# Optimization experiments

Hardware: AMD Instinct MI355X
Metric: run time of the kernel (lower is better)

Reference implementation:

```python
import jax, jax.numpy as jnp
import numpy as np

N_NODES = 100000
N_EDGES = 1600000
IN_F, HID_F, OUT_F = 64, 64, 32


def setup_inputs() -> dict:
    key = jax.random.key(0)
    k = jax.random.split(key, 6)
    features = jax.random.normal(k[0], (N_NODES, IN_F), dtype=jnp.float32)
    src = jax.random.randint(k[1], (N_EDGES,), 0, N_NODES, dtype=jnp.int32)
    dst = jax.random.randint(k[2], (N_EDGES,), 0, N_NODES, dtype=jnp.int32)
    # Linear params (Kaiming-uniform-ish scale)
    W1 = jax.random.normal(k[3], (IN_F, HID_F), dtype=jnp.float32) / np.sqrt(IN_F)
    b1 = jnp.zeros((HID_F,), dtype=jnp.float32)
    W2 = jax.random.normal(k[4], (HID_F, OUT_F), dtype=jnp.float32) / np.sqrt(HID_F)
    b2 = jnp.zeros((OUT_F,), dtype=jnp.float32)
    return {"features": features, "src": src, "dst": dst,
            "W1": W1, "b1": b1, "W2": W2, "b2": b2}


def _graph_conv(src, dst, n_nodes, h, W, b):
    # copy_u + sum: scatter-add source features into destination nodes (SpMM)
    agg = jax.ops.segment_sum(h[src], dst, num_segments=n_nodes)
    return agg @ W + b


def reference(features, src, dst, W1, b1, W2, b2):
    n = features.shape[0]
    h = jax.nn.relu(_graph_conv(src, dst, n, features, W1, b1))
    h = _graph_conv(src, dst, n, h, W2, b2)
    return h
```

## Files before the change

kernel.cpp:

```cpp
#include <hip/hip_runtime.h>

#define N_NODES 100000
#define N_EDGES 1600000
#define NB 782
#define CAP 3072
#define EPB 8192
#define NP1 196
#define CVB 200
#define YP 72
#define AP 72

typedef __attribute__((ext_vector_type(8))) short bhalf8;
typedef __attribute__((ext_vector_type(4))) float f32x4;

__device__ __forceinline__ unsigned short bf16r(float f) {
    unsigned u = __float_as_uint(f);
    unsigned r = (u >> 16) & 1;
    return (unsigned short)((u + 0x7fffu + r) >> 16);
}
__device__ __forceinline__ unsigned pk2(float a, float b) {
    return (unsigned)bf16r(a) | ((unsigned)bf16r(b) << 16);
}
__device__ __forceinline__ float bl(unsigned u) { return __uint_as_float(u << 16); }
__device__ __forceinline__ float bh(unsigned u) { return __uint_as_float(u & 0xffff0000u); }

__global__ __launch_bounds__(512) void prep(const float4* __restrict__ X4,
                                            uint2* __restrict__ Xb,
                                            const int* __restrict__ src,
                                            const int* __restrict__ dst,
                                            int* __restrict__ gcur,
                                            unsigned* __restrict__ ebuf) {
    __shared__ int h[NB];
    __shared__ int lo[NB];
    __shared__ int cur[NB];
    __shared__ int wsum[8];
    __shared__ unsigned stage[EPB];
    __shared__ unsigned short bid[EPB];
    int t = threadIdx.x, lane = t & 63, wid = t >> 6;
    if (blockIdx.x >= NP1) {
        for (int i = (blockIdx.x - NP1) * 512 + t; i < N_NODES * 16; i += CVB * 512) {
            float4 v = X4[i];
            uint2 o; o.x = pk2(v.x, v.y); o.y = pk2(v.z, v.w);
            Xb[i] = o;
        }
        return;
    }
    int e0 = blockIdx.x * EPB;
    int eN = N_EDGES - e0; if (eN > EPB) eN = EPB;
    for (int b = t; b < NB; b += 512) h[b] = 0;
    __syncthreads();
    for (int i = t; i < eN; i += 512) atomicAdd(&h[dst[e0 + i] >> 7], 1);
    __syncthreads();
    int i0 = 2 * t, i1 = i0 + 1;
    int v0 = (i0 < NB) ? h[i0] : 0;
    int v1 = (i1 < NB) ? h[i1] : 0;
    int ps = v0 + v1, s = ps;
    for (int o = 1; o < 64; o <<= 1) {
        int u = __shfl_up(s, o);
        if (lane >= o) s += u;
    }
    if (lane == 63) wsum[wid] = s;
    __syncthreads();
    int wofs = 0;
    for (int w = 0; w < wid; w++) wofs += wsum[w];
    int excl = wofs + s - ps;
    if (i0 < NB) lo[i0] = excl;
    if (i1 < NB) lo[i1] = excl + v0;
    __syncthreads();
    for (int b = t; b < NB; b += 512) {
        int hb = h[b];
        int ofs = hb ? atomicAdd(&gcur[b], hb) : 0;
        h[b] = b * CAP + ofs - lo[b];
        cur[b] = lo[b];
    }
    __syncthreads();
    for (int i = t; i < eN; i += 512) {
        int sd = src[e0 + i], dd = dst[e0 + i];
        int b = dd >> 7;
        int r = atomicAdd(&cur[b], 1);
        stage[r] = ((unsigned)sd << 7) | (unsigned)(dd & 127);
        bid[r] = (unsigned short)b;
    }
    __syncthreads();
    for (int i = t; i < eN; i += 512)
        ebuf[h[bid[i]] + i] = stage[i];
}

__global__ __launch_bounds__(512) void bucket1(
    const unsigned* __restrict__ ebuf, const int* __restrict__ gcur,
    const uint4* __restrict__ Xb4,
    const float* __restrict__ W1, const float* __restrict__ b1,
    const float* __restrict__ W2,
    unsigned short* __restrict__ Zb) {
    __shared__ int hh[128], nodeoff[129], scv[128];
    __shared__ unsigned short agg[128 * AP];
    __shared__ int pool[3456];
    int* stg = pool;
    unsigned short* sW1t = (unsigned short*)pool;
    unsigned short* sW2t = (unsigned short*)(pool + 2304);

    int b = blockIdx.x, t = threadIdx.x;
    int base = b * CAP, cnt = gcur[b];
    int lane = t & 63, wid = t >> 6;
    if (t < 128) hh[t] = 0;
    __syncthreads();
    unsigned ev[6]; int ek = 0;
    for (int i = t; i < cnt; i += 512) {
        unsigned v = ebuf[base + i];
        ev[ek++] = v;
        atomicAdd(&hh[v & 127], 1);
    }
    __syncthreads();
    if (wid == 0) {
        int v0 = hh[2 * lane], v1 = hh[2 * lane + 1];
        int ps = v0 + v1, s = ps;
        for (int o = 1; o < 64; o <<= 1) {
            int u = __shfl_up(s, o);
            if (lane >= o) s += u;
        }
        int excl = s - ps;
        nodeoff[2 * lane] = excl;
        nodeoff[2 * lane + 1] = excl + v0;
    }
    __syncthreads();
    if (t < 128) scv[t] = nodeoff[t];
    __syncthreads();
    for (int k = 0; k < ek; k++) {
        unsigned v = ev[k];
        int r = atomicAdd(&scv[v & 127], 1);
        stg[r] = (int)(v >> 7);
    }
    __syncthreads();

    int il = lane & 7, g = lane >> 3;
#pragma unroll
    for (int half = 0; half < 2; half++) {
        int nl = wid * 16 + half * 8 + g;
        int s0 = nodeoff[nl], d = hh[nl];
        float a0 = 0.f, a1 = 0.f, a2 = 0.f, a3 = 0.f;
        float a4 = 0.f, a5 = 0.f, a6 = 0.f, a7 = 0.f;
        int j = 0;
        for (; j + 3 < d; j += 4) {
            int sa = stg[s0 + j], sb = stg[s0 + j + 1];
            int sc = stg[s0 + j + 2], sd = stg[s0 + j + 3];
            uint4 va = Xb4[sa * 8 + il], vb = Xb4[sb * 8 + il];
            uint4 vc = Xb4[sc * 8 + il], vd = Xb4[sd * 8 + il];
            a0 += bl(va.x) + bl(vb.x) + bl(vc.x) + bl(vd.x);
            a1 += bh(va.x) + bh(vb.x) + bh(vc.x) + bh(vd.x);
            a2 += bl(va.y) + bl(vb.y) + bl(vc.y) + bl(vd.y);
            a3 += bh(va.y) + bh(vb.y) + bh(vc.y) + bh(vd.y);
            a4 += bl(va.z) + bl(vb.z) + bl(vc.z) + bl(vd.z);
            a5 += bh(va.z) + bh(vb.z) + bh(vc.z) + bh(vd.z);
            a6 += bl(va.w) + bl(vb.w) + bl(vc.w) + bl(vd.w);
            a7 += bh(va.w) + bh(vb.w) + bh(vc.w) + bh(vd.w);
        }
        for (; j < d; j++) {
            int sa = stg[s0 + j];
            uint4 va = Xb4[sa * 8 + il];
            a0 += bl(va.x); a1 += bh(va.x); a2 += bl(va.y); a3 += bh(va.y);
            a4 += bl(va.z); a5 += bh(va.z); a6 += bl(va.w); a7 += bh(va.w);
        }
        uint4 o;
        o.x = pk2(a0, a1); o.y = pk2(a2, a3);
        o.z = pk2(a4, a5); o.w = pk2(a6, a7);
        *(uint4*)&agg[nl * AP + il * 8] = o;
    }
    __syncthreads();

    for (int i = t; i < 64 * 64; i += 512) {
        int k = i >> 6, hc = i & 63;
        sW1t[hc * YP + k] = bf16r(W1[k * 64 + hc]);
    }
    for (int i = t; i < 64 * 32; i += 512) {
        int k = i >> 5, oc = i & 31;
        sW2t[oc * YP + k] = bf16r(W2[k * 32 + oc]);
    }
    __syncthreads();

    {
        int m = lane & 15, quad = lane >> 4;
        int nl = wid * 16 + m;
        int node = b * 128 + nl;
        bhalf8 Bc0 = *(const bhalf8*)&agg[nl * AP + quad * 8];
        bhalf8 Bc1 = *(const bhalf8*)&agg[nl * AP + 32 + quad * 8];
        unsigned short* ys = &agg[nl * AP];
#pragma unroll
        for (int tile = 0; tile < 4; tile++) {
            f32x4 a;
#pragma unroll
            for (int r = 0; r < 4; r++) a[r] = b1[tile * 16 + quad * 4 + r];
            bhalf8 A0 = *(const bhalf8*)&sW1t[(tile * 16 + m) * YP + quad * 8];
            bhalf8 A1 = *(const bhalf8*)&sW1t[(tile * 16 + m) * YP + 32 + quad * 8];
            a = __builtin_amdgcn_mfma_f32_16x16x32_bf16(A0, Bc0, a, 0, 0, 0);
            a = __builtin_amdgcn_mfma_f32_16x16x32_bf16(A1, Bc1, a, 0, 0, 0);
            float y0 = a[0] > 0.f ? a[0] : 0.f, y1 = a[1] > 0.f ? a[1] : 0.f;
            float y2 = a[2] > 0.f ? a[2] : 0.f, y3 = a[3] > 0.f ? a[3] : 0.f;
            uint2 o; o.x = pk2(y0, y1); o.y = pk2(y2, y3);
            *(uint2*)&ys[tile * 16 + quad * 4] = o;
        }
        __asm__ __volatile__("s_waitcnt lgkmcnt(0)" ::: "memory");
        union { bhalf8 v; uint2 u2[2]; } Y0, Y1;
        Y0.u2[0] = *(uint2*)&ys[quad * 8];
        Y0.u2[1] = *(uint2*)&ys[quad * 8 + 4];
        Y1.u2[0] = *(uint2*)&ys[32 + quad * 8];
        Y1.u2[1] = *(uint2*)&ys[32 + quad * 8 + 4];
#pragma unroll
        for (int tile = 0; tile < 2; tile++) {
            bhalf8 A0 = *(const bhalf8*)&sW2t[(tile * 16 + m) * YP + quad * 8];
            bhalf8 A1 = *(const bhalf8*)&sW2t[(tile * 16 + m) * YP + 32 + quad * 8];
            f32x4 z = {0.f, 0.f, 0.f, 0.f};
            z = __builtin_amdgcn_mfma_f32_16x16x32_bf16(A0, Y0.v, z, 0, 0, 0);
            z = __builtin_amdgcn_mfma_f32_16x16x32_bf16(A1, Y1.v, z, 0, 0, 0);
            if (node < N_NODES) {
                uint2 o; o.x = pk2(z[0], z[1]); o.y = pk2(z[2], z[3]);
                *(uint2*)&Zb[(size_t)node * 32 + tile * 16 + quad * 4] = o;
            }
        }
    }
}

__global__ __launch_bounds__(512) void bucket2(
    const unsigned* __restrict__ ebuf, const int* __restrict__ gcur,
    const uint4* __restrict__ Zb4,
    const float* __restrict__ b2, float4* __restrict__ out4) {
    __shared__ int hh[128], nodeoff[129], scv[128];
    __shared__ int stg[CAP];
    int b = blockIdx.x, t = threadIdx.x;
    int base = b * CAP, cnt = gcur[b];
    int lane = t & 63, wid = t >> 6;
    if (t < 128) hh[t] = 0;
    __syncthreads();
    unsigned ev[6]; int ek = 0;
    for (int i = t; i < cnt; i += 512) {
        unsigned v = ebuf[base + i];
        ev[ek++] = v;
        atomicAdd(&hh[v & 127], 1);
    }
    __syncthreads();
    if (wid == 0) {
        int v0 = hh[2 * lane], v1 = hh[2 * lane + 1];
        int ps = v0 + v1, s = ps;
        for (int o = 1; o < 64; o <<= 1) {
            int u = __shfl_up(s, o);
            if (lane >= o) s += u;
        }
        int excl = s - ps;
        nodeoff[2 * lane] = excl;
        nodeoff[2 * lane + 1] = excl + v0;
    }
    __syncthreads();
    if (t < 128) scv[t] = nodeoff[t];
    __syncthreads();
    for (int k = 0; k < ek; k++) {
        unsigned v = ev[k];
        int r = atomicAdd(&scv[v & 127], 1);
        stg[r] = (int)(v >> 7);
    }
    __syncthreads();

    int il = lane & 3, g = lane >> 2;
    int nl = wid * 16 + g;
    int s0 = nodeoff[nl], d = hh[nl];
    float a0 = 0.f, a1 = 0.f, a2 = 0.f, a3 = 0.f;
    float a4 = 0.f, a5 = 0.f, a6 = 0.f, a7 = 0.f;
    int j = 0;
    for (; j + 3 < d; j += 4) {
        int sa = stg[s0 + j], sb = stg[s0 + j + 1];
        int sc = stg[s0 + j + 2], sd = stg[s0 + j + 3];
        uint4 va = Zb4[sa * 4 + il], vb = Zb4[sb * 4 + il];
        uint4 vc = Zb4[sc * 4 + il], vd = Zb4[sd * 4 + il];
        a0 += bl(va.x) + bl(vb.x) + bl(vc.x) + bl(vd.x);
        a1 += bh(va.x) + bh(vb.x) + bh(vc.x) + bh(vd.x);
        a2 += bl(va.y) + bl(vb.y) + bl(vc.y) + bl(vd.y);
        a3 += bh(va.y) + bh(vb.y) + bh(vc.y) + bh(vd.y);
        a4 += bl(va.z) + bl(vb.z) + bl(vc.z) + bl(vd.z);
        a5 += bh(va.z) + bh(vb.z) + bh(vc.z) + bh(vd.z);
        a6 += bl(va.w) + bl(vb.w) + bl(vc.w) + bl(vd.w);
        a7 += bh(va.w) + bh(vb.w) + bh(vc.w) + bh(vd.w);
    }
    for (; j < d; j++) {
        int sa = stg[s0 + j];
        uint4 va = Zb4[sa * 4 + il];
        a0 += bl(va.x); a1 += bh(va.x); a2 += bl(va.y); a3 += bh(va.y);
        a4 += bl(va.z); a5 += bh(va.z); a6 += bl(va.w); a7 += bh(va.w);
    }
    int node = b * 128 + nl;
    if (node < N_NODES) {
        float4 bbA = ((const float4*)b2)[il * 2];
        float4 bbB = ((const float4*)b2)[il * 2 + 1];
        float4 oA, oB;
        oA.x = a0 + bbA.x; oA.y = a1 + bbA.y; oA.z = a2 + bbA.z; oA.w = a3 + bbA.w;
        oB.x = a4 + bbB.x; oB.y = a5 + bbB.y; oB.z = a6 + bbB.z; oB.w = a7 + bbB.w;
        out4[node * 8 + il * 2] = oA;
        out4[node * 8 + il * 2 + 1] = oB;
    }
}

extern "C" void kernel_launch(void* const* d_in, const int* in_sizes, int n_in,
                              void* d_out, int out_size, void* d_ws, size_t ws_size,
                              hipStream_t stream) {
    const float* features = (const float*)d_in[0];
    const int*   src      = (const int*)d_in[1];
    const int*   dst      = (const int*)d_in[2];
    const float* W1       = (const float*)d_in[3];
    const float* b1       = (const float*)d_in[4];
    const float* W2       = (const float*)d_in[5];
    const float* b2       = (const float*)d_in[6];

    char* p = (char*)d_ws;
    int* gcur = (int*)p;           p += 1024 * 4;
    unsigned* ebuf = (unsigned*)p; p += (size_t)NB * CAP * 4;
    uint2* Xb = (uint2*)p;         p += (size_t)N_NODES * 64 * 2;
    unsigned short* Zb = (unsigned short*)p; p += (size_t)N_NODES * 32 * 2;

    hipMemsetAsync(gcur, 0, NB * sizeof(int), stream);
    prep<<<NP1 + CVB, 512, 0, stream>>>((const float4*)features, Xb, src, dst, gcur, ebuf);
    bucket1<<<NB, 512, 0, stream>>>(ebuf, gcur, (const uint4*)Xb, W1, b1, W2, Zb);
    bucket2<<<NB, 512, 0, stream>>>(ebuf, gcur, (const uint4*)Zb, b2, (float4*)d_out);
}
```

Measured before the change: 160.3 us.

## Persist per-node CSR from layer one and reuse it in a lean layer-two gather

bucket1 now writes the per-bucket sorted source list (csr) plus per-node offsets and degrees to global memory. The second layer becomes a simple gather kernel with 256-thread blocks that reads this CSR directly. This removes the duplicate histogram, scan and local sort that bucket2 used to run. The cost is an extra global write of about 1.6M indices plus the offset and degree arrays, and no shared-memory staging of the neighbor indices in layer two.

Result: slower. 165.6 us (+3.3%).

```diff
diff --git a/kernel.cpp b/kernel.cpp
--- a/kernel.cpp
+++ b/kernel.cpp
@@ -91,6 +91,7 @@
     const uint4* __restrict__ Xb4,
     const float* __restrict__ W1, const float* __restrict__ b1,
     const float* __restrict__ W2,
+    int* __restrict__ off, int* __restrict__ deg, int* __restrict__ csr,
     unsigned short* __restrict__ Zb) {
     __shared__ int hh[128], nodeoff[129], scv[128];
     __shared__ unsigned short agg[128 * AP];
@@ -123,7 +124,11 @@
         nodeoff[2 * lane + 1] = excl + v0;
     }
     __syncthreads();
-    if (t < 128) scv[t] = nodeoff[t];
+    if (t < 128) {
+        int n = b * 128 + t;
+        if (n < N_NODES) { off[n] = base + nodeoff[t]; deg[n] = hh[t]; }
+        scv[t] = nodeoff[t];
+    }
     __syncthreads();
     for (int k = 0; k < ek; k++) {
         unsigned v = ev[k];
@@ -131,6 +136,7 @@
         stg[r] = (int)(v >> 7);
     }
     __syncthreads();
+    for (int i = t; i < cnt; i += 512) csr[base + i] = stg[i];
 
     int il = lane & 7, g = lane >> 3;
 #pragma unroll
@@ -219,80 +225,45 @@
     }
 }
 
-__global__ __launch_bounds__(512) void bucket2(
-    const unsigned* __restrict__ ebuf, const int* __restrict__ gcur,
-    const uint4* __restrict__ Zb4,
+__global__ __launch_bounds__(256) void gather2(
+    const uint4* __restrict__ Zb4, const int* __restrict__ off,
+    const int* __restrict__ deg, const int* __restrict__ csr,
     const float* __restrict__ b2, float4* __restrict__ out4) {
-    __shared__ int hh[128], nodeoff[129], scv[128];
-    __shared__ int stg[CAP];
-    int b = blockIdx.x, t = threadIdx.x;
-    int base = b * CAP, cnt = gcur[b];
-    int lane = t & 63, wid = t >> 6;
-    if (t < 128) hh[t] = 0;
-    __syncthreads();
-    unsigned ev[6]; int ek = 0;
-    for (int i = t; i < cnt; i += 512) {
-        unsigned v = ebuf[base + i];
-        ev[ek++] = v;
-        atomicAdd(&hh[v & 127], 1);
-    }
-    __syncthreads();
-    if (wid == 0) {
-        int v0 = hh[2 * lane], v1 = hh[2 * lane + 1];
-        int ps = v0 + v1, s = ps;
-        for (int o = 1; o < 64; o <<= 1) {
-            int u = __shfl_up(s, o);
-            if (lane >= o) s += u;
-        }
-        int excl = s - ps;
-        nodeoff[2 * lane] = excl;
-        nodeoff[2 * lane + 1] = excl + v0;
-    }
-    __syncthreads();
-    if (t < 128) scv[t] = nodeoff[t];
-    __syncthreads();
-    for (int k = 0; k < ek; k++) {
-        unsigned v = ev[k];
-        int r = atomicAdd(&scv[v & 127], 1);
-        stg[r] = (int)(v >> 7);
-    }
-    __syncthreads();
-
+    int t = threadIdx.x, lane = t & 63, wid = t >> 6;
     int il = lane & 3, g = lane >> 2;
-    int nl = wid * 16 + g;
-    int s0 = nodeoff[nl], d = hh[nl];
-    float a0 = 0.f, a1 = 0.f, a2 = 0.f, a3 = 0.f;
-    float a4 = 0.f, a5 = 0.f, a6 = 0.f, a7 = 0.f;
-    int j = 0;
-    for (; j + 3 < d; j += 4) {
-        int sa = stg[s0 + j], sb = stg[s0 + j + 1];
-        int sc = stg[s0 + j + 2], sd = stg[s0 + j + 3];
-        uint4 va = Zb4[sa * 4 + il], vb = Zb4[sb * 4 + il];
-        uint4 vc = Zb4[sc * 4 + il], vd = Zb4[sd * 4 + il];
-        a0 += bl(va.x) + bl(vb.x) + bl(vc.x) + bl(vd.x);
-        a1 += bh(va.x) + bh(vb.x) + bh(vc.x) + bh(vd.x);
-        a2 += bl(va.y) + bl(vb.y) + bl(vc.y) + bl(vd.y);
-        a3 += bh(va.y) + bh(vb.y) + bh(vc.y) + bh(vd.y);
-        a4 += bl(va.z) + bl(vb.z) + bl(vc.z) + bl(vd.z);
-        a5 += bh(va.z) + bh(vb.z) + bh(vc.z) + bh(vd.z);
-        a6 += bl(va.w) + bl(vb.w) + bl(vc.w) + bl(vd.w);
-        a7 += bh(va.w) + bh(vb.w) + bh(vc.w) + bh(vd.w);
-    }
-    for (; j < d; j++) {
-        int sa = stg[s0 + j];
-        uint4 va = Zb4[sa * 4 + il];
-        a0 += bl(va.x); a1 += bh(va.x); a2 += bl(va.y); a3 += bh(va.y);
-        a4 += bl(va.z); a5 += bh(va.z); a6 += bl(va.w); a7 += bh(va.w);
-    }
-    int node = b * 128 + nl;
-    if (node < N_NODES) {
-        float4 bbA = ((const float4*)b2)[il * 2];
-        float4 bbB = ((const float4*)b2)[il * 2 + 1];
+    float4 bbA = ((const float4*)b2)[il * 2];
+    float4 bbB = ((const float4*)b2)[il * 2 + 1];
+    int n0 = blockIdx.x * 64 + wid * 16 + g, stride = gridDim.x * 64;
+    for (int n = n0; n < N_NODES; n += stride) {
+        int s0 = off[n], d = deg[n];
+        float a0 = 0.f, a1 = 0.f, a2 = 0.f, a3 = 0.f;
+        float a4 = 0.f, a5 = 0.f, a6 = 0.f, a7 = 0.f;
+        int j = 0;
+        for (; j + 3 < d; j += 4) {
+            int sa = csr[s0 + j], sb = csr[s0 + j + 1];
+            int sc = csr[s0 + j + 2], sd = csr[s0 + j + 3];
+            uint4 va = Zb4[sa * 4 + il], vb = Zb4[sb * 4 + il];
+            uint4 vc = Zb4[sc * 4 + il], vd = Zb4[sd * 4 + il];
+            a0 += bl(va.x) + bl(vb.x) + bl(vc.x) + bl(vd.x);
+            a1 += bh(va.x) + bh(vb.x) + bh(vc.x) + bh(vd.x);
+            a2 += bl(va.y) + bl(vb.y) + bl(vc.y) + bl(vd.y);
+            a3 += bh(va.y) + bh(vb.y) + bh(vc.y) + bh(vd.y);
+            a4 += bl(va.z) + bl(vb.z) + bl(vc.z) + bl(vd.z);
+            a5 += bh(va.z) + bh(vb.z) + bh(vc.z) + bh(vd.z);
+            a6 += bl(va.w) + bl(vb.w) + bl(vc.w) + bl(vd.w);
+            a7 += bh(va.w) + bh(vb.w) + bh(vc.w) + bh(vd.w);
+        }
+        for (; j < d; j++) {
+            int sa = csr[s0 + j];
+            uint4 va = Zb4[sa * 4 + il];
+            a0 += bl(va.x); a1 += bh(va.x); a2 += bl(va.y); a3 += bh(va.y);
+            a4 += bl(va.z); a5 += bh(va.z); a6 += bl(va.w); a7 += bh(va.w);
+        }
         float4 oA, oB;
         oA.x = a0 + bbA.x; oA.y = a1 + bbA.y; oA.z = a2 + bbA.z; oA.w = a3 + bbA.w;
         oB.x = a4 + bbB.x; oB.y = a5 + bbB.y; oB.z = a6 + bbB.z; oB.w = a7 + bbB.w;
-        out4[node * 8 + il * 2] = oA;
-        out4[node * 8 + il * 2 + 1] = oB;
+        out4[n * 8 + il * 2] = oA;
+        out4[n * 8 + il * 2 + 1] = oB;
     }
 }
 
@@ -309,12 +280,16 @@
 
     char* p = (char*)d_ws;
     int* gcur = (int*)p;           p += 1024 * 4;
+    int* off  = (int*)p;           p += ((size_t)N_NODES * 4 + 255) / 256 * 256;
+    int* deg  = (int*)p;           p += ((size_t)N_NODES * 4 + 255) / 256 * 256;
     unsigned* ebuf = (unsigned*)p; p += (size_t)NB * CAP * 4;
+    int* csr  = (int*)p;           p += (size_t)NB * CAP * 4;
     uint2* Xb = (uint2*)p;         p += (size_t)N_NODES * 64 * 2;
     unsigned short* Zb = (unsigned short*)p; p += (size_t)N_NODES * 32 * 2;
 
     hipMemsetAsync(gcur, 0, NB * sizeof(int), stream);
     prep<<<NP1 + CVB, 512, 0, stream>>>((const float4*)features, Xb, src, dst, gcur, ebuf);
-    bucket1<<<NB, 512, 0, stream>>>(ebuf, gcur, (const uint4*)Xb, W1, b1, W2, Zb);
-    bucket2<<<NB, 512, 0, stream>>>(ebuf, gcur, (const uint4*)Zb, b2, (float4*)d_out);
-}
+    bucket1<<<NB, 512, 0, stream>>>(ebuf, gcur, (const uint4*)Xb, W1, b1, W2,
+                                    off, deg, csr, Zb);
+    gather2<<<1563, 256, 0, stream>>>((const uint4*)Zb, off, deg, csr, b2, (float4*)d_out);
+}
```
